# Performance work log

Hardware: AMD Instinct MI355X
Metric: run time of the kernel (lower is better)

Reference implementation:

```python
import jax, jax.numpy as jnp
import numpy as np

T, D, E = 8192, 1024, 64
CAPACITY_FACTOR = 2.0
CAP = int(CAPACITY_FACTOR * np.ceil(T / E))  # 256 (training-mode capacity)
EPS = 1e-4


def setup_inputs() -> dict:
    key = jax.random.key(0)
    k1, k2, k3 = jax.random.split(key, 3)
    x = jax.random.normal(k1, (T, D), dtype=jnp.float32)
    W_red = jax.random.normal(k2, (D, 4), dtype=jnp.float32) * 0.02
    centroids = jax.random.normal(k3, (E, 4), dtype=jnp.float32)
    return {"x": x, "W_red": W_red, "centroids": centroids}


def reference(x, W_red, centroids):
    # dim reduction (nn.Linear(model_dim, 4, bias=False))
    red = x @ W_red  # [T, 4]
    # cosine logits: centroids are L2-normalized inside _cosine (the in-place
    # 1.5/norm rescale of the parameter cancels under F.normalize)
    c = centroids.astype(jnp.float32)
    cn = c / jnp.maximum(jnp.linalg.norm(c, axis=1, keepdims=True), EPS)
    logits = red.astype(jnp.float32) @ cn.T  # [T, E]
    # _make_finite
    finite = jnp.isfinite(logits)
    fmin = jnp.min(jnp.where(finite, logits, jnp.inf))
    logits = jnp.where(finite, logits, fmin)

    gates = jax.nn.softmax(logits, axis=1)                 # [T, E]
    idx1 = jnp.argmax(gates, axis=1)                       # [T]
    mask1 = jax.nn.one_hot(idx1, E, dtype=gates.dtype)     # [T, E]
    expert_counts = jnp.sum(mask1, axis=0).astype(jnp.int32)  # metadata

    gates1_s = 1.5 * jnp.sum(gates * mask1, axis=1)        # [T]
    loc1 = jnp.cumsum(mask1, axis=0) - 1.0                 # positions within expert

    me = jnp.mean(gates, axis=0)
    ce = jnp.mean(mask1, axis=0)
    l_aux = jnp.mean(me * ce) * (E * E)

    mask1 = mask1 * (loc1 < CAP).astype(mask1.dtype)       # drop overflow tokens
    loc1_s = jnp.sum(loc1 * mask1, axis=1).astype(jnp.int32)  # [T]
    gates1 = gates1_s[:, None] * mask1                     # [T, E]
    loc_sc = jax.nn.one_hot(loc1_s, CAP, dtype=gates1.dtype)  # [T, CAP]
    combine = gates1[:, :, None] * loc_sc[:, None, :]      # [T, E, CAP]
    dispatch_mask = combine != 0
    return (l_aux, combine.astype(x.dtype), dispatch_mask, expert_counts)
```

## Files before the change

kernel.cpp:

```cpp
#include <hip/hip_runtime.h>

#define T 8192
#define D 1024
#define E 64
#define CAP 256

typedef float f32x4 __attribute__((ext_vector_type(4)));

#define TEC ((size_t)134217728)
#define C_OFF   ((size_t)1)
#define M_OFF   ((size_t)1 + TEC)
#define CNT_OFF ((size_t)1 + 2 * TEC)

__global__ __launch_bounds__(256) void kA_gate_fill(
    const float* __restrict__ x, const float* __restrict__ Wred,
    const float* __restrict__ cent, int* __restrict__ idx1,
    float* __restrict__ g15, float* __restrict__ Sg, int* __restrict__ bc,
    float* __restrict__ out)
{
    __shared__ float wcol[4 * D];
    __shared__ float cn[E * 4];
    __shared__ float sg[E];
    const int tid = threadIdx.x;

    for (int i = tid; i < 4 * D; i += 256) {
        int d = i >> 2, c = i & 3;
        wcol[c * D + d] = Wred[i];
    }
    if (tid < E) {
        float c0 = cent[tid * 4 + 0];
        float c1 = cent[tid * 4 + 1];
        float c2 = cent[tid * 4 + 2];
        float c3 = cent[tid * 4 + 3];
        float n = fmaxf(sqrtf(c0 * c0 + c1 * c1 + c2 * c2 + c3 * c3), 1e-4f);
        cn[tid * 4 + 0] = c0 / n;
        cn[tid * 4 + 1] = c1 / n;
        cn[tid * 4 + 2] = c2 / n;
        cn[tid * 4 + 3] = c3 / n;
        sg[tid] = 0.0f;
    }
    __syncthreads();

    const int wave = tid >> 6, lane = tid & 63;
    const int t = blockIdx.x * 4 + wave;
    {
        const float* xr = x + (size_t)t * D;
        float a0 = 0.f, a1 = 0.f, a2 = 0.f, a3 = 0.f;
        #pragma unroll
        for (int k = 0; k < 16; ++k) {
            int d = k * 64 + lane;
            float xv = xr[d];
            a0 += xv * wcol[d];
            a1 += xv * wcol[D + d];
            a2 += xv * wcol[2 * D + d];
            a3 += xv * wcol[3 * D + d];
        }
        #pragma unroll
        for (int off = 32; off; off >>= 1) {
            a0 += __shfl_xor(a0, off);
            a1 += __shfl_xor(a1, off);
            a2 += __shfl_xor(a2, off);
            a3 += __shfl_xor(a3, off);
        }
        float logit = a0 * cn[lane * 4 + 0] + a1 * cn[lane * 4 + 1]
                    + a2 * cn[lane * 4 + 2] + a3 * cn[lane * 4 + 3];
        float m = logit;
        #pragma unroll
        for (int off = 32; off; off >>= 1) m = fmaxf(m, __shfl_xor(m, off));
        unsigned long long ball = __ballot(logit == m);
        int amax = __ffsll(ball) - 1;
        float ev = expf(logit - m);
        float s = ev;
        #pragma unroll
        for (int off = 32; off; off >>= 1) s += __shfl_xor(s, off);
        atomicAdd(&sg[lane], ev / s);
        if (lane == 0) {
            idx1[t] = amax;
            g15[t] = 1.5f / s;
            atomicAdd(&bc[(t >> 8) * E + amax], 1);
        }
    }
    __syncthreads();
    if (tid < E) atomicAdd(&Sg[tid], sg[tid]);

    const f32x4 z4 = {0.f, 0.f, 0.f, 0.f};
    f32x4* __restrict__ base = (f32x4*)(out + 4);
    const size_t b0 = (size_t)blockIdx.x * 32768;
    #pragma unroll 4
    for (int k = 0; k < 128; ++k) {
        size_t fi = b0 + (size_t)k * 256 + tid;
        if (fi < (size_t)67108863) base[fi] = z4;
    }
    if (blockIdx.x == 0 && tid < 4) {
        if (tid < 3) out[1 + tid] = 0.f;
        else         out[2 * TEC] = 0.f;
    }
}

__global__ __launch_bounds__(256) void k5_prefix_patch(
    const int* __restrict__ idx1, const float* __restrict__ g15,
    const int* __restrict__ bc, const float* __restrict__ Sg,
    float* __restrict__ out)
{
    __shared__ int pfe[E];
    __shared__ int cwf[256];
    const int tid = threadIdx.x;
    const int chunk = blockIdx.x;
    const int t = chunk * 256 + tid;
    const int e = idx1[t];

    if (tid < E) {
        int run = 0;
        for (int b = 0; b < chunk; ++b) run += bc[b * E + tid];
        pfe[tid] = run;
    }
    cwf[tid] = 0;
    __syncthreads();

    const int wave = tid >> 6, lane = tid & 63;
    unsigned long long same = ~0ull;
    #pragma unroll
    for (int b = 0; b < 6; ++b) {
        unsigned long long bal = __ballot(((e >> b) & 1) != 0);
        same &= ((e >> b) & 1) ? bal : ~bal;
    }
    const unsigned long long below = ((unsigned long long)1 << lane) - 1ull;
    const int rank_in_wave = __popcll(same & below);
    if ((same & below) == 0ull) cwf[wave * E + e] = __popcll(same);
    __syncthreads();

    int rank = pfe[e] + rank_in_wave;
    if (wave > 0) rank += cwf[0 * E + e];
    if (wave > 1) rank += cwf[1 * E + e];
    if (wave > 2) rank += cwf[2 * E + e];

    if (rank < CAP) {
        const size_t row = (size_t)t * (E * CAP) + (size_t)e * CAP + rank;
        out[C_OFF + row] = g15[t];
        out[M_OFF + row] = 1.0f;
    }

    if (chunk == 31 && tid < E) {
        int total = pfe[tid] + bc[31 * E + tid];
        out[CNT_OFF + tid] = (float)total;
        float v = Sg[tid] * (float)total;
        #pragma unroll
        for (int off = 32; off; off >>= 1) v += __shfl_xor(v, off);
        if (tid == 0) out[0] = v * ((float)E / ((float)T * (float)T));
    }
}

extern "C" void kernel_launch(void* const* d_in, const int* in_sizes, int n_in,
                              void* d_out, int out_size, void* d_ws, size_t ws_size,
                              hipStream_t stream)
{
    const float* x    = (const float*)d_in[0];
    const float* Wred = (const float*)d_in[1];
    const float* cent = (const float*)d_in[2];
    float* out = (float*)d_out;

    char* ws = (char*)d_ws;
    int*   idx1 = (int*)ws;
    float* g15  = (float*)(ws + 32768);
    float* Sg   = (float*)(ws + 65536);
    int*   bc   = (int*)(ws + 65536 + 256);

    (void)hipMemsetAsync(Sg, 0, 256 + 32 * E * sizeof(int), stream);

    kA_gate_fill<<<2048, 256, 0, stream>>>(x, Wred, cent, idx1, g15, Sg, bc, out);
    k5_prefix_patch<<<32, 256, 0, stream>>>(idx1, g15, bc, Sg, out);
}
```

Before: 1.093 ms.

## Replace fused in-kernel zero fill with hipMemset and vectorize gate kernel

Removes the 1 GB output zero-fill from the gating kernel and uses a runtime memset on the whole output instead. The gate kernel now uses float4 loads of x and W, and each block handles 16 tokens over 512 blocks. This gives up the overlap of the fill with gate compute and relies on the driver's memset bandwidth, which could be faster or slower than the hand-written store loop. out_size is assumed to be in bytes.

```diff
diff --git a/kernel.cpp b/kernel.cpp
--- a/kernel.cpp
+++ b/kernel.cpp
@@ -12,11 +12,10 @@
 #define M_OFF   ((size_t)1 + TEC)
 #define CNT_OFF ((size_t)1 + 2 * TEC)
 
-__global__ __launch_bounds__(256) void kA_gate_fill(
+__global__ __launch_bounds__(256) void k1_gate(
     const float* __restrict__ x, const float* __restrict__ Wred,
     const float* __restrict__ cent, int* __restrict__ idx1,
-    float* __restrict__ g15, float* __restrict__ Sg, int* __restrict__ bc,
-    float* __restrict__ out)
+    float* __restrict__ g15, float* __restrict__ Sg, int* __restrict__ bc)
 {
     __shared__ float wcol[4 * D];
     __shared__ float cn[E * 4];
@@ -41,19 +40,24 @@
     }
     __syncthreads();
 
+    const f32x4* __restrict__ wc4 = (const f32x4*)wcol;
     const int wave = tid >> 6, lane = tid & 63;
-    const int t = blockIdx.x * 4 + wave;
-    {
-        const float* xr = x + (size_t)t * D;
+    for (int it = 0; it < 4; ++it) {
+        const int t = blockIdx.x * 16 + it * 4 + wave;
+        const f32x4* __restrict__ xr4 = (const f32x4*)(x + (size_t)t * D);
         float a0 = 0.f, a1 = 0.f, a2 = 0.f, a3 = 0.f;
         #pragma unroll
-        for (int k = 0; k < 16; ++k) {
-            int d = k * 64 + lane;
-            float xv = xr[d];
-            a0 += xv * wcol[d];
-            a1 += xv * wcol[D + d];
-            a2 += xv * wcol[2 * D + d];
-            a3 += xv * wcol[3 * D + d];
+        for (int k = 0; k < 4; ++k) {
+            const int i = k * 64 + lane;
+            const f32x4 xv = xr4[i];
+            const f32x4 w0 = wc4[0 * 256 + i];
+            const f32x4 w1 = wc4[1 * 256 + i];
+            const f32x4 w2 = wc4[2 * 256 + i];
+            const f32x4 w3 = wc4[3 * 256 + i];
+            a0 += xv[0] * w0[0] + xv[1] * w0[1] + xv[2] * w0[2] + xv[3] * w0[3];
+            a1 += xv[0] * w1[0] + xv[1] * w1[1] + xv[2] * w1[2] + xv[3] * w1[3];
+            a2 += xv[0] * w2[0] + xv[1] * w2[1] + xv[2] * w2[2] + xv[3] * w2[3];
+            a3 += xv[0] * w3[0] + xv[1] * w3[1] + xv[2] * w3[2] + xv[3] * w3[3];
         }
         #pragma unroll
         for (int off = 32; off; off >>= 1) {
@@ -82,19 +86,6 @@
     }
     __syncthreads();
     if (tid < E) atomicAdd(&Sg[tid], sg[tid]);
-
-    const f32x4 z4 = {0.f, 0.f, 0.f, 0.f};
-    f32x4* __restrict__ base = (f32x4*)(out + 4);
-    const size_t b0 = (size_t)blockIdx.x * 32768;
-    #pragma unroll 4
-    for (int k = 0; k < 128; ++k) {
-        size_t fi = b0 + (size_t)k * 256 + tid;
-        if (fi < (size_t)67108863) base[fi] = z4;
-    }
-    if (blockIdx.x == 0 && tid < 4) {
-        if (tid < 3) out[1 + tid] = 0.f;
-        else         out[2 * TEC] = 0.f;
-    }
 }
 
 __global__ __launch_bounds__(256) void k5_prefix_patch(
@@ -165,8 +156,9 @@
     float* Sg   = (float*)(ws + 65536);
     int*   bc   = (int*)(ws + 65536 + 256);
 
+    (void)hipMemsetAsync(d_out, 0, (size_t)out_size, stream);
     (void)hipMemsetAsync(Sg, 0, 256 + 32 * E * sizeof(int), stream);
 
-    kA_gate_fill<<<2048, 256, 0, stream>>>(x, Wred, cent, idx1, g15, Sg, bc, out);
+    k1_gate<<<512, 256, 0, stream>>>(x, Wred, cent, idx1, g15, Sg, bc);
     k5_prefix_patch<<<32, 256, 0, stream>>>(idx1, g15, bc, Sg, out);
 }
```

Measured after the change: 932.8 us (median of 2 runs). 14.6% less time.
